# Kernel optimization log

Hardware: AMD Instinct MI355X
Metric: run time of the kernel (lower is better)

Reference implementation:

```python
import jax, jax.numpy as jnp
import numpy as np
from jax import lax

NUM_HEADS = 8
EPS = 1e-12  # F.normalize default eps


def _l2norm(t):
    # F.normalize(t, dim=-1): t / max(||t||_2, eps)
    n = jnp.sqrt(jnp.sum(t * t, axis=-1, keepdims=True))
    return t / jnp.maximum(n, EPS)


def setup_inputs() -> dict:
    key = jax.random.key(0)
    k1, k2, k3, k4 = jax.random.split(key, 4)
    b, c, h, w = 16, 384, 64, 64
    x = jax.random.normal(k1, (b, c, h, w), dtype=jnp.float32)
    # 1x1 conv weights stored as (out, in); depthwise 3x3 as (3c, 1, 3, 3)
    w_qkv = jax.random.normal(k2, (3 * c, c), dtype=jnp.float32) * (1.0 / np.sqrt(c))
    w_dw = jax.random.normal(k3, (3 * c, 1, 3, 3), dtype=jnp.float32) * (1.0 / 3.0)
    w_proj = jax.random.normal(k4, (c, c), dtype=jnp.float32) * (1.0 / np.sqrt(c))
    temperature = jnp.ones((1, NUM_HEADS, 1, 1), dtype=jnp.float32)
    return {"x": x, "w_qkv": w_qkv, "w_dw": w_dw, "w_proj": w_proj,
            "temperature": temperature}


def reference(x, w_qkv, w_dw, w_proj, temperature):
    b, c, h, w = x.shape
    hw = h * w
    d = c // NUM_HEADS  # per-head channel dim

    # 1x1 pointwise conv: (b,c,h,w) x (3c,c) -> (b,3c,h,w)
    qkv = jnp.einsum('bchw,oc->bohw', x, w_qkv)
    # depthwise 3x3 conv, groups = 3c, padding SAME, no bias
    qkv = lax.conv_general_dilated(
        qkv, w_dw, window_strides=(1, 1), padding='SAME',
        feature_group_count=3 * c,
        dimension_numbers=('NCHW', 'OIHW', 'NCHW'))

    q, k, v = jnp.split(qkv, 3, axis=1)
    q = q.reshape(b, NUM_HEADS, d, hw)
    k = k.reshape(b, NUM_HEADS, d, hw)
    v = v.reshape(b, NUM_HEADS, d, hw)

    q = _l2norm(q)
    k = _l2norm(k)

    # transposed (channel) attention: scores over channel dim, (b,H,d,d)
    scores = jnp.einsum('bhdn,bhen->bhde', q, k) * temperature
    attn = jax.nn.softmax(scores, axis=-1)

    out = jnp.einsum('bhde,bhen->bhdn', attn, v).reshape(b, c, h, w)
    out = jnp.einsum('bchw,oc->bohw', out, w_proj)
    return out
```

## Files before the change

kernel.cpp:

```cpp
#include <hip/hip_runtime.h>
#include <hip/hip_bf16.h>
#include <math.h>

#define B_   16
#define C_   384
#define C3_  1152
#define HW_  4096
#define NH_  8
#define D_   48

typedef _Float16 f16x8 __attribute__((ext_vector_type(8)));
typedef _Float16 f16x4 __attribute__((ext_vector_type(4)));
typedef _Float16 f16x2 __attribute__((ext_vector_type(2)));
typedef float    f32x4 __attribute__((ext_vector_type(4)));

#define ASM_VMCNT(n) asm volatile("s_waitcnt vmcnt(" #n ")" ::: "memory")

__global__ __launch_bounds__(256) void conv_w_f16(
    const float* __restrict__ w, _Float16* __restrict__ wh, int n4)
{
    int i = blockIdx.x * 256 + threadIdx.x;
    if (i < n4) {
        float4 v = *(const float4*)&w[(size_t)i * 4];
        f16x4 h = { (_Float16)v.x, (_Float16)v.y, (_Float16)v.z, (_Float16)v.w };
        *(f16x4*)&wh[(size_t)i * 4] = h;
    }
}

__global__ __launch_bounds__(256) void transpose_to_f16(
    const float* __restrict__ x, _Float16* __restrict__ xt)
{
    const int b  = blockIdx.z;
    const int k0 = blockIdx.y * 64;
    const int n0 = blockIdx.x * 64;
    __shared__ float sm[64][65];
    const float* xb = x + (size_t)b * C_ * HW_;
    _Float16* xtb = xt + (size_t)b * HW_ * C_;
    const int t = threadIdx.x;
    #pragma unroll
    for (int i = 0; i < 4; ++i) {
        int row = (t >> 4) + i * 16;
        int col = (t & 15) * 4;
        float4 v = *(const float4*)&xb[(size_t)(k0 + row) * HW_ + n0 + col];
        sm[row][col] = v.x; sm[row][col+1] = v.y; sm[row][col+2] = v.z; sm[row][col+3] = v.w;
    }
    __syncthreads();
    #pragma unroll
    for (int i = 0; i < 2; ++i) {
        int nl = (t >> 3) + i * 32;
        int ks = (t & 7) * 8;
        f16x8 h;
        #pragma unroll
        for (int j = 0; j < 8; ++j) h[j] = (_Float16)sm[ks + j][nl];
        *(f16x8*)&xtb[(size_t)(n0 + nl) * C_ + k0 + ks] = h;
    }
}

template<int M, bool F32OUT>
__global__ __launch_bounds__(256, 2) void mfma_gemm(
    const _Float16* __restrict__ Wb,
    const _Float16* __restrict__ XT,
    void* __restrict__ Cv, long long xstride, long long cstride)
{
    constexpr int K = 384;
    constexpr int BK = 32;
    constexpr int NSTEP = K / BK;
    constexpr int MB = M / 128;
    __shared__ _Float16 lds[3][(128 + 256) * BK];

    const int nwg = MB * 16 * B_;
    const int cpx = nwg >> 3;
    const int bid = blockIdx.x;
    const int L   = (bid & 7) * cpx + (bid >> 3);
    const int m0  = (L % MB) * 128;
    const int nb  = L / MB;
    const int n0  = (nb & 15) * 256;
    const int b   = nb >> 4;

    const _Float16* __restrict__ XTb = XT + (size_t)b * xstride;
    const int t = threadIdx.x;
    const int l = t & 63, w = t >> 6;
    const int frow = l & 15, kseg16 = l >> 4;

    auto stage = [&](int d, int kt) {
        const int kk = kt * BK;
        #pragma unroll
        for (int i = 0; i < 2; ++i) {
            const int u = i * 256 + t;
            const int row = u >> 2, slot = u & 3;
            const int scol = slot ^ (row & 3) ^ ((row >> 2) & 1);
            const _Float16* ga = Wb + (size_t)(m0 + row) * K + kk + scol * 8;
            __builtin_amdgcn_global_load_lds(
                (const __attribute__((address_space(1))) void*)ga,
                (__attribute__((address_space(3))) void*)((char*)&lds[d][0] + u * 16),
                16, 0, 0);
        }
        #pragma unroll
        for (int i = 0; i < 4; ++i) {
            const int u = i * 256 + t;
            const int row = u >> 2, slot = u & 3;
            const int scol = slot ^ (row & 3) ^ ((row >> 2) & 1);
            const _Float16* gb = XTb + (size_t)(n0 + row) * K + kk + scol * 8;
            __builtin_amdgcn_global_load_lds(
                (const __attribute__((address_space(1))) void*)gb,
                (__attribute__((address_space(3))) void*)((char*)&lds[d][0] + 8192 + u * 16),
                16, 0, 0);
        }
    };

    f32x4 acc[8][4] = {};

    stage(0, 0); stage(1, 1); stage(2, 2);
    #pragma unroll
    for (int kt = 0; kt < NSTEP; ++kt) {
        const int cur = kt % 3;
        if (kt <= 9)       { ASM_VMCNT(12); }
        else if (kt == 10) { ASM_VMCNT(6); }
        else               { ASM_VMCNT(0); }
        __builtin_amdgcn_sched_barrier(0);
        __builtin_amdgcn_s_barrier();
        __builtin_amdgcn_sched_barrier(0);
        f16x8 af[8], bfr[4];
        #pragma unroll
        for (int mi = 0; mi < 8; ++mi) {
            const int rA = mi * 16 + frow;
            const int cs = kseg16 ^ (rA & 3) ^ ((rA >> 2) & 1);
            af[mi] = *(const f16x8*)&lds[cur][rA * 32 + cs * 8];
        }
        #pragma unroll
        for (int ni = 0; ni < 4; ++ni) {
            const int rB = w * 64 + ni * 16 + frow;
            const int cs = kseg16 ^ (rB & 3) ^ ((rB >> 2) & 1);
            bfr[ni] = *(const f16x8*)&lds[cur][4096 + rB * 32 + cs * 8];
        }
        __builtin_amdgcn_s_setprio(1);
        #pragma unroll
        for (int mi = 0; mi < 8; ++mi)
            #pragma unroll
            for (int ni = 0; ni < 4; ++ni)
                acc[mi][ni] = __builtin_amdgcn_mfma_f32_16x16x32_f16(
                    bfr[ni], af[mi], acc[mi][ni], 0, 0, 0);
        __builtin_amdgcn_s_setprio(0);
        asm volatile("s_waitcnt lgkmcnt(0)" ::: "memory");
        __builtin_amdgcn_sched_barrier(0);
        __builtin_amdgcn_s_barrier();
        if (kt + 3 < NSTEP) stage(cur, kt + 3);
    }
    const int pxl = (l >> 4) * 4;
    const int chl = l & 15;
    if constexpr (F32OUT) {
        float* Co = (float*)Cv + (size_t)b * cstride;
        #pragma unroll
        for (int mi = 0; mi < 8; ++mi)
            #pragma unroll
            for (int ni = 0; ni < 4; ++ni)
                *(f32x4*)&Co[(size_t)(m0 + mi * 16 + chl) * HW_
                             + n0 + w * 64 + ni * 16 + pxl] = acc[mi][ni];
    } else {
        _Float16* Co = (_Float16*)Cv + (size_t)b * cstride;
        #pragma unroll
        for (int mi = 0; mi < 8; ++mi)
            #pragma unroll
            for (int ni = 0; ni < 4; ++ni) {
                f16x4 h;
                #pragma unroll
                for (int r = 0; r < 4; ++r) h[r] = (_Float16)acc[mi][ni][r];
                *(f16x4*)&Co[(size_t)(m0 + mi * 16 + chl) * HW_
                             + n0 + w * 64 + ni * 16 + pxl] = h;
            }
    }
}

__global__ __launch_bounds__(256) void dwconv_norm(
    _Float16* __restrict__ buf, const float* __restrict__ wdw,
    float* __restrict__ nqinv, float* __restrict__ nkinv)
{
    const int plane = blockIdx.x;
    const int ch = plane % C3_, b = plane / C3_;
    __shared__ _Float16 smh[64 * 72];
    __shared__ float wsum[4];
    _Float16* g = buf + (size_t)plane * HW_;
    const int t = threadIdx.x;
    #pragma unroll
    for (int i = 0; i < 2; ++i) {
        const int u = i * 256 + t;
        f16x8 v = *(const f16x8*)&g[u * 8];
        *(f16x8*)&smh[(u >> 3) * 72 + (u & 7) * 8] = v;
    }
    float w[9];
    #pragma unroll
    for (int j = 0; j < 9; ++j) w[j] = wdw[ch * 9 + j];
    __syncthreads();
    float ssq = 0.f;
    #pragma unroll
    for (int i = 0; i < 2; ++i) {
        const int u = i * 256 + t;
        const int y = u >> 3, c0 = (u & 7) * 8;
        float r[3][10];
        #pragma unroll
        for (int dy = 0; dy < 3; ++dy) {
            const int yy = y + dy - 1;
            if (yy < 0 || yy > 63) {
                #pragma unroll
                for (int j = 0; j < 10; ++j) r[dy][j] = 0.f;
            } else {
                f16x8 v = *(const f16x8*)&smh[yy * 72 + c0];
                #pragma unroll
                for (int j = 0; j < 8; ++j) r[dy][j + 1] = (float)v[j];
                r[dy][0] = (c0 > 0)  ? (float)smh[yy * 72 + c0 - 1] : 0.f;
                r[dy][9] = (c0 < 56) ? (float)smh[yy * 72 + c0 + 8] : 0.f;
            }
        }
        f16x8 o;
        #pragma unroll
        for (int j = 0; j < 8; ++j) {
            float s = 0.f;
            #pragma unroll
            for (int dy = 0; dy < 3; ++dy)
                #pragma unroll
                for (int dx = 0; dx < 3; ++dx)
                    s = fmaf(w[dy * 3 + dx], r[dy][j + dx], s);
            o[j] = (_Float16)s;
            ssq = fmaf(s, s, ssq);
        }
        *(f16x8*)&g[u * 8] = o;
    }
    if (ch < 2 * C_) {
        #pragma unroll
        for (int m = 1; m < 64; m <<= 1) ssq += __shfl_xor(ssq, m);
        if ((t & 63) == 0) wsum[t >> 6] = ssq;
        __syncthreads();
        if (t == 0) {
            float tot = wsum[0] + wsum[1] + wsum[2] + wsum[3];
            float inv = 1.f / fmaxf(sqrtf(tot), 1e-12f);
            (ch < C_ ? nqinv : nkinv)[b * C_ + (ch % C_)] = inv;
        }
    }
}

__global__ __launch_bounds__(256) void scores_mfma(
    const _Float16* __restrict__ buf, float* __restrict__ sp)
{
    const int bh = blockIdx.x;
    const int ks = blockIdx.y;
    const int b = bh >> 3, h = bh & 7;
    const _Float16* qbase = buf + ((size_t)b * C3_ + (size_t)h * D_) * HW_;
    const _Float16* kbase = qbase + (size_t)C_ * HW_;
    const int t = threadIdx.x, l = t & 63, w = t >> 6;
    const int frow = l & 15, kseg = (l >> 4) * 8;
    const int p0 = ks * 1024 + w * 256;

    f32x4 acc[3][3] = {};
    #pragma unroll 2
    for (int st = 0; st < 8; ++st) {
        const int p = p0 + st * 32 + kseg;
        f16x8 qf[3], kf[3];
        #pragma unroll
        for (int mi = 0; mi < 3; ++mi)
            qf[mi] = *(const f16x8*)&qbase[(size_t)(mi * 16 + frow) * HW_ + p];
        #pragma unroll
        for (int ni = 0; ni < 3; ++ni)
            kf[ni] = *(const f16x8*)&kbase[(size_t)(ni * 16 + frow) * HW_ + p];
        #pragma unroll
        for (int mi = 0; mi < 3; ++mi)
            #pragma unroll
            for (int ni = 0; ni < 3; ++ni)
                acc[mi][ni] = __builtin_amdgcn_mfma_f32_16x16x32_f16(
                    qf[mi], kf[ni], acc[mi][ni], 0, 0, 0);
    }
    __shared__ float red[4][D_ * D_];
    #pragma unroll
    for (int mi = 0; mi < 3; ++mi)
        #pragma unroll
        for (int ni = 0; ni < 3; ++ni)
            #pragma unroll
            for (int r = 0; r < 4; ++r)
                red[w][(mi * 16 + (l >> 4) * 4 + r) * D_ + ni * 16 + (l & 15)] =
                    acc[mi][ni][r];
    __syncthreads();
    float* out = sp + ((size_t)ks * 128 + bh) * (D_ * D_);
    const float* rf = &red[0][0];
    for (int i = t; i < D_ * D_; i += 256)
        out[i] = rf[i] + rf[2304 + i] + rf[4608 + i] + rf[6912 + i];
}

__global__ __launch_bounds__(256) void softmax_k(
    const float* __restrict__ sp, const float* __restrict__ nqinv,
    const float* __restrict__ nkinv, const float* __restrict__ temp,
    float* __restrict__ attn)
{
    const int row = blockIdx.x * 4 + (threadIdx.x >> 6);
    const int bh = row / D_, d = row % D_;
    const int h = bh & 7;
    const int e = threadIdx.x & 63;
    float s = -INFINITY;
    if (e < D_) {
        float raw = 0.f;
        #pragma unroll
        for (int ks = 0; ks < 4; ++ks)
            raw += sp[((size_t)ks * 128 + bh) * (D_ * D_) + d * D_ + e];
        s = raw * nqinv[bh * D_ + d] * nkinv[bh * D_ + e] * temp[h];
    }
    float m = s;
    #pragma unroll
    for (int off = 1; off < 64; off <<= 1) m = fmaxf(m, __shfl_xor(m, off));
    float p = (e < D_) ? expf(s - m) : 0.f;
    float sum = p;
    #pragma unroll
    for (int off = 1; off < 64; off <<= 1) sum += __shfl_xor(sum, off);
    if (e < D_) attn[(size_t)bh * (D_ * D_) + d * D_ + e] = p / sum;
}

__global__ __launch_bounds__(256) void pv_kernel(
    _Float16* __restrict__ buf, const float* __restrict__ attn)
{
    const int b = blockIdx.z, h = blockIdx.y;
    const int p0 = blockIdx.x * 512 + threadIdx.x * 2;
    __shared__ float a4[48][48];
    const float* ab = attn + ((size_t)b * 8 + h) * (D_ * D_);
    for (int i = threadIdx.x; i < D_ * D_; i += 256) ((float*)a4)[i] = ab[i];
    __syncthreads();
    const _Float16* vbase = buf + ((size_t)b * C3_ + 2 * C_ + (size_t)h * D_) * HW_;
    float2 acc[48];
    #pragma unroll
    for (int d = 0; d < 48; ++d) { acc[d].x = 0.f; acc[d].y = 0.f; }
    #pragma unroll 1
    for (int e4 = 0; e4 < 12; ++e4) {
        float2 vv[4];
        #pragma unroll
        for (int j = 0; j < 4; ++j) {
            f16x2 h2 = *(const f16x2*)&vbase[(size_t)(e4 * 4 + j) * HW_ + p0];
            vv[j].x = (float)h2[0]; vv[j].y = (float)h2[1];
        }
        #pragma unroll
        for (int d = 0; d < 48; ++d) {
            float4 a = *(const float4*)&a4[d][e4 * 4];
            acc[d].x = fmaf(a.x, vv[0].x, fmaf(a.y, vv[1].x, fmaf(a.z, vv[2].x, fmaf(a.w, vv[3].x, acc[d].x))));
            acc[d].y = fmaf(a.x, vv[0].y, fmaf(a.y, vv[1].y, fmaf(a.z, vv[2].y, fmaf(a.w, vv[3].y, acc[d].y))));
        }
    }
    _Float16* xt2b = buf + (size_t)b * C3_ * HW_;
    #pragma unroll
    for (int px = 0; px < 2; ++px) {
        f16x8 tmp[6];
        #pragma unroll
        for (int d = 0; d < 48; ++d) tmp[d >> 3][d & 7] = (_Float16)(px ? acc[d].y : acc[d].x);
        f16x8* dst = (f16x8*)&xt2b[(size_t)(p0 + px) * C_ + h * D_];
        #pragma unroll
        for (int j = 0; j < 6; ++j) dst[j] = tmp[j];
    }
}

extern "C" void kernel_launch(void* const* d_in, const int* in_sizes, int n_in,
                              void* d_out, int out_size, void* d_ws, size_t ws_size,
                              hipStream_t stream)
{
    const float* x      = (const float*)d_in[0];
    const float* w_qkv  = (const float*)d_in[1];
    const float* w_dw   = (const float*)d_in[2];
    const float* w_proj = (const float*)d_in[3];
    const float* temp   = (const float*)d_in[4];
    float* out = (float*)d_out;

    _Float16* buf = (_Float16*)d_ws;
    float* nqinv = (float*)(buf + (size_t)B_ * C3_ * HW_);
    float* nkinv = nqinv + 6144;
    float* sp    = nkinv + 6144;
    float* attn  = sp + (size_t)4 * 128 * D_ * D_;
    _Float16* wqkv_h  = (_Float16*)(attn + (size_t)128 * D_ * D_);
    _Float16* wproj_h = wqkv_h + (size_t)C3_ * C_;
    _Float16* xt1     = wproj_h + (size_t)C_ * C_;

    conv_w_f16<<<(C3_ * C_ / 4 + 255) / 256, 256, 0, stream>>>(w_qkv, wqkv_h, C3_ * C_ / 4);
    conv_w_f16<<<(C_ * C_ / 4 + 255) / 256, 256, 0, stream>>>(w_proj, wproj_h, C_ * C_ / 4);
    transpose_to_f16<<<dim3(64, 6, 16), 256, 0, stream>>>(x, xt1);

    mfma_gemm<C3_, false><<<dim3(9 * 16 * 16), 256, 0, stream>>>(
        wqkv_h, xt1, buf, (long long)HW_ * C_, (long long)C3_ * HW_);

    dwconv_norm<<<B_ * C3_, 256, 0, stream>>>(buf, w_dw, nqinv, nkinv);

    scores_mfma<<<dim3(128, 4), 256, 0, stream>>>(buf, sp);

    softmax_k<<<1536, 256, 0, stream>>>(sp, nqinv, nkinv, temp, attn);

    pv_kernel<<<dim3(8, 8, 16), 256, 0, stream>>>(buf, attn);

    mfma_gemm<C_, true><<<dim3(3 * 16 * 16), 256, 0, stream>>>(
        wproj_h, buf, out, (long long)C3_ * HW_, (long long)C_ * HW_);
}
```

Measured before the change: 296.6 us.

## Load GEMM A operand directly to registers and merge weight-conversion kernels

The GEMM stops staging the weight (A) tile through LDS. Each thread now loads its A fragments straight from global memory into double-buffered registers one k-step ahead, while only the activation (B) tile goes through a triple-buffered LDS ring with prefetch distance 2 and a single barrier per step. This is meant to cut LDS traffic and one barrier per iteration, at the cost of more VGPRs and uncoalesced global reads of A. The two fp32-to-fp16 weight conversion kernels are also merged into one launch to save launch overhead.

```diff
diff --git a/kernel.cpp b/kernel.cpp
--- a/kernel.cpp
+++ b/kernel.cpp
@@ -16,15 +16,20 @@
 
 #define ASM_VMCNT(n) asm volatile("s_waitcnt vmcnt(" #n ")" ::: "memory")
 
-__global__ __launch_bounds__(256) void conv_w_f16(
-    const float* __restrict__ w, _Float16* __restrict__ wh, int n4)
-{
+__global__ __launch_bounds__(256) void conv_w_all(
+    const float* __restrict__ wqkv, const float* __restrict__ wproj,
+    _Float16* __restrict__ oq, _Float16* __restrict__ op)
+{
+    const int nq = C3_ * C_ / 4;
+    const int np = C_ * C_ / 4;
     int i = blockIdx.x * 256 + threadIdx.x;
-    if (i < n4) {
-        float4 v = *(const float4*)&w[(size_t)i * 4];
-        f16x4 h = { (_Float16)v.x, (_Float16)v.y, (_Float16)v.z, (_Float16)v.w };
-        *(f16x4*)&wh[(size_t)i * 4] = h;
-    }
+    const float* src; _Float16* dst; int j;
+    if (i < nq) { src = wqkv; dst = oq; j = i; }
+    else if (i < nq + np) { src = wproj; dst = op; j = i - nq; }
+    else return;
+    float4 v = *(const float4*)&src[(size_t)j * 4];
+    f16x4 h = { (_Float16)v.x, (_Float16)v.y, (_Float16)v.z, (_Float16)v.w };
+    *(f16x4*)&dst[(size_t)j * 4] = h;
 }
 
 __global__ __launch_bounds__(256) void transpose_to_f16(
@@ -66,7 +71,7 @@
     constexpr int BK = 32;
     constexpr int NSTEP = K / BK;
     constexpr int MB = M / 128;
-    __shared__ _Float16 lds[3][(128 + 256) * BK];
+    __shared__ _Float16 Bsh[3][256 * BK];
 
     const int nwg = MB * 16 * B_;
     const int cpx = nwg >> 3;
@@ -82,19 +87,13 @@
     const int l = t & 63, w = t >> 6;
     const int frow = l & 15, kseg16 = l >> 4;
 
-    auto stage = [&](int d, int kt) {
+    const _Float16* ap[8];
+    #pragma unroll
+    for (int mi = 0; mi < 8; ++mi)
+        ap[mi] = &Wb[(size_t)(m0 + mi * 16 + frow) * K + kseg16 * 8];
+
+    auto stageB = [&](int d, int kt) {
         const int kk = kt * BK;
-        #pragma unroll
-        for (int i = 0; i < 2; ++i) {
-            const int u = i * 256 + t;
-            const int row = u >> 2, slot = u & 3;
-            const int scol = slot ^ (row & 3) ^ ((row >> 2) & 1);
-            const _Float16* ga = Wb + (size_t)(m0 + row) * K + kk + scol * 8;
-            __builtin_amdgcn_global_load_lds(
-                (const __attribute__((address_space(1))) void*)ga,
-                (__attribute__((address_space(3))) void*)((char*)&lds[d][0] + u * 16),
-                16, 0, 0);
-        }
         #pragma unroll
         for (int i = 0; i < 4; ++i) {
             const int u = i * 256 + t;
@@ -103,48 +102,51 @@
             const _Float16* gb = XTb + (size_t)(n0 + row) * K + kk + scol * 8;
             __builtin_amdgcn_global_load_lds(
                 (const __attribute__((address_space(1))) void*)gb,
-                (__attribute__((address_space(3))) void*)((char*)&lds[d][0] + 8192 + u * 16),
+                (__attribute__((address_space(3))) void*)((char*)&Bsh[d][0] + u * 16),
                 16, 0, 0);
         }
     };
 
     f32x4 acc[8][4] = {};
-
-    stage(0, 0); stage(1, 1); stage(2, 2);
+    f16x8 afA[8], afB[8];
+
+    stageB(0, 0);
+    stageB(1, 1);
+    #pragma unroll
+    for (int mi = 0; mi < 8; ++mi) afA[mi] = *(const f16x8*)(ap[mi]);
+
     #pragma unroll
     for (int kt = 0; kt < NSTEP; ++kt) {
         const int cur = kt % 3;
-        if (kt <= 9)       { ASM_VMCNT(12); }
-        else if (kt == 10) { ASM_VMCNT(6); }
-        else               { ASM_VMCNT(0); }
+        if (kt == NSTEP - 1) { ASM_VMCNT(8); } else { ASM_VMCNT(12); }
         __builtin_amdgcn_sched_barrier(0);
         __builtin_amdgcn_s_barrier();
         __builtin_amdgcn_sched_barrier(0);
-        f16x8 af[8], bfr[4];
-        #pragma unroll
-        for (int mi = 0; mi < 8; ++mi) {
-            const int rA = mi * 16 + frow;
-            const int cs = kseg16 ^ (rA & 3) ^ ((rA >> 2) & 1);
-            af[mi] = *(const f16x8*)&lds[cur][rA * 32 + cs * 8];
-        }
+        if (kt + 2 < NSTEP) stageB((kt + 2) % 3, kt + 2);
+        if (kt + 1 < NSTEP) {
+            f16x8* afn = (kt & 1) ? afA : afB;
+            #pragma unroll
+            for (int mi = 0; mi < 8; ++mi)
+                afn[mi] = *(const f16x8*)(ap[mi] + (kt + 1) * BK);
+        }
+        f16x8 bfr[4];
         #pragma unroll
         for (int ni = 0; ni < 4; ++ni) {
             const int rB = w * 64 + ni * 16 + frow;
             const int cs = kseg16 ^ (rB & 3) ^ ((rB >> 2) & 1);
-            bfr[ni] = *(const f16x8*)&lds[cur][4096 + rB * 32 + cs * 8];
-        }
+            bfr[ni] = *(const f16x8*)&Bsh[cur][rB * 32 + cs * 8];
+        }
+        const f16x8* afc = (kt & 1) ? afB : afA;
         __builtin_amdgcn_s_setprio(1);
         #pragma unroll
         for (int mi = 0; mi < 8; ++mi)
             #pragma unroll
             for (int ni = 0; ni < 4; ++ni)
                 acc[mi][ni] = __builtin_amdgcn_mfma_f32_16x16x32_f16(
-                    bfr[ni], af[mi], acc[mi][ni], 0, 0, 0);
+                    bfr[ni], afc[mi], acc[mi][ni], 0, 0, 0);
         __builtin_amdgcn_s_setprio(0);
         asm volatile("s_waitcnt lgkmcnt(0)" ::: "memory");
         __builtin_amdgcn_sched_barrier(0);
-        __builtin_amdgcn_s_barrier();
-        if (kt + 3 < NSTEP) stage(cur, kt + 3);
     }
     const int pxl = (l >> 4) * 4;
     const int chl = l & 15;
@@ -371,8 +373,8 @@
     _Float16* wproj_h = wqkv_h + (size_t)C3_ * C_;
     _Float16* xt1     = wproj_h + (size_t)C_ * C_;
 
-    conv_w_f16<<<(C3_ * C_ / 4 + 255) / 256, 256, 0, stream>>>(w_qkv, wqkv_h, C3_ * C_ / 4);
-    conv_w_f16<<<(C_ * C_ / 4 + 255) / 256, 256, 0, stream>>>(w_proj, wproj_h, C_ * C_ / 4);
+    conv_w_all<<<(C3_ * C_ / 4 + C_ * C_ / 4 + 255) / 256, 256, 0, stream>>>(
+        w_qkv, w_proj, wqkv_h, wproj_h);
     transpose_to_f16<<<dim3(64, 6, 16), 256, 0, stream>>>(x, xt1);
 
     mfma_gemm<C3_, false><<<dim3(9 * 16 * 16), 256, 0, stream>>>(
```

New measurement: 370.7 us. 1.25x slower.
